# Kernel tuning notes

Hardware: AMD Instinct MI355X
Metric: run time of the kernel (lower is better)

## Reference

```python
import jax, jax.numpy as jnp
import numpy as np

C = 32
H = 8

def _layernorm(x, scale, bias, eps=1e-5):
    mu = jnp.mean(x, axis=-1, keepdims=True)
    var = jnp.mean(jnp.square(x - mu), axis=-1, keepdims=True)
    return (x - mu) * jax.lax.rsqrt(var + eps) * scale + bias


def setup_inputs() -> dict:
    key = jax.random.key(0)
    ks = jax.random.split(key, 10)
    B, s, i, j = 1, 128, 256, 256
    m = jax.random.normal(ks[0], (B, s, i, C), dtype=jnp.float32)
    z = jax.random.normal(ks[1], (B, i, j, C), dtype=jnp.float32)
    sd = 1.0 / np.sqrt(C)
    return {
        "m": m,
        "z": z,
        "ln_scale": jnp.ones((C,), jnp.float32),
        "ln_bias": jnp.zeros((C,), jnp.float32),
        "lnb_scale": jnp.ones((C,), jnp.float32),
        "lnb_bias": jnp.zeros((C,), jnp.float32),
        "wq": jax.random.normal(ks[2], (C, C * H), jnp.float32) * sd,
        "wk": jax.random.normal(ks[3], (C, C * H), jnp.float32) * sd,
        "wv": jax.random.normal(ks[4], (C, C * H), jnp.float32) * sd,
        "wb": jax.random.normal(ks[5], (C, H), jnp.float32) * sd,
        "wg": jax.random.normal(ks[6], (C, C * H), jnp.float32) * sd,
        "wo": jax.random.normal(ks[7], (C * H, C), jnp.float32) * (1.0 / np.sqrt(C * H)),
        "bo": jnp.zeros((C,), jnp.float32),
    }


def reference(m, z, ln_scale, ln_bias, lnb_scale, lnb_bias, wq, wk, wv, wb, wg, wo, bo):
    B, s, i, _ = m.shape
    j = z.shape[2]
    mn = _layernorm(m, ln_scale, ln_bias)                      # (B,s,i,c)
    q = (mn @ wq).reshape(B, s, i, H, C)                        # (B,s,i,h,c)
    k = (mn @ wk).reshape(B, s, i, H, C)
    v = (mn @ wv).reshape(B, s, i, H, C)
    gate = jax.nn.sigmoid(mn @ wg).reshape(B, s, i, H, C)       # (B,s,i,h,c)
    b = (_layernorm(z, lnb_scale, lnb_bias) @ wb)               # (B,i,j,h)
    a = jnp.einsum('bsihc,bsjhc->bsijh', q, k) * (C ** -0.5) + b[:, None]
    a = jax.nn.softmax(a, axis=-2)                              # softmax over j
    o = gate * jnp.einsum('bsijh,bsjhc->bsihc', a, v)
    o = o.reshape(B, s, i, H * C)
    return o @ wo + bo
```

## Files before the change

kernel.cpp:

```cpp
#include <hip/hip_runtime.h>

constexpr int NC = 32;
constexpr int NH = 8;
constexpr int NS = 128;
constexpr int NI = 256;
constexpr int NJ = 256;
constexpr float LN_EPS = 1e-5f;
constexpr float QSCALE = 0.17677669529663687f;
constexpr float LOG2E  = 1.4426950408889634f;

typedef __bf16 bf16x8 __attribute__((ext_vector_type(8)));
typedef __bf16 bf16x2 __attribute__((ext_vector_type(2)));
typedef float floatx4 __attribute__((ext_vector_type(4)));

__device__ __forceinline__ float fexp2(float x) {
#if __has_builtin(__builtin_amdgcn_exp2f)
    return __builtin_amdgcn_exp2f(x);
#else
    return exp2f(x);
#endif
}
__device__ __forceinline__ float frcp(float x) {
#if __has_builtin(__builtin_amdgcn_rcpf)
    return __builtin_amdgcn_rcpf(x);
#else
    return 1.0f / x;
#endif
}
__device__ __forceinline__ unsigned pk2c(float a, float b) {
    union { bf16x2 v; unsigned u; } c;
    c.v = bf16x2{(__bf16)a, (__bf16)b};
    return c.u;
}

__device__ __forceinline__ int qkOff(int row, int chunk) {
    return row * 32 + ((chunk ^ ((row >> 1) & 3)) << 3);
}
__device__ __forceinline__ int vOff(int c, int chunk) {
    return c * 256 + ((chunk ^ (c & 7)) << 3);
}
__device__ __forceinline__ int pOff(int wbase, int row, int chunk) {
    return wbase + row * 32 + ((chunk ^ ((row >> 1) & 3)) << 3);
}

__global__ __launch_bounds__(256) void biasprep_kernel(
    const float* __restrict__ z, const float* __restrict__ lnb_s,
    const float* __restrict__ lnb_b, const float* __restrict__ wb,
    const float* __restrict__ wq, const float* __restrict__ wk,
    const float* __restrict__ wv, const float* __restrict__ wg,
    const float* __restrict__ wo,
    float* __restrict__ bias32, unsigned short* __restrict__ wprep,
    unsigned short* __restrict__ wofrag)
{
    const int b = blockIdx.x;
    const int t = threadIdx.x;
    if (b < 256) {
        __shared__ float zL[256 * 33];
        const float4* src = (const float4*)(z + (size_t)b * NJ * NC);
#pragma unroll
        for (int k = 0; k < 8; ++k) {
            int idx = t + 256 * k;
            float4 v = src[idx];
            int f = idx * 4;
            int j = f >> 5, c = f & 31;
            zL[j * 33 + c]     = v.x; zL[j * 33 + c + 1] = v.y;
            zL[j * 33 + c + 2] = v.z; zL[j * 33 + c + 3] = v.w;
        }
        __syncthreads();

        float x[NC];
#pragma unroll
        for (int c = 0; c < NC; ++c) x[c] = zL[t * 33 + c];
        float mu = 0.f;
#pragma unroll
        for (int c = 0; c < NC; ++c) mu += x[c];
        mu *= (1.0f / NC);
        float var = 0.f;
#pragma unroll
        for (int c = 0; c < NC; ++c) { float d = x[c] - mu; var += d * d; }
        var *= (1.0f / NC);
        float rs = rsqrtf(var + LN_EPS);
        float acc[NH];
#pragma unroll
        for (int h = 0; h < NH; ++h) acc[h] = 0.f;
#pragma unroll
        for (int c = 0; c < NC; ++c) {
            float xn = (x[c] - mu) * rs * lnb_s[c] + lnb_b[c];
#pragma unroll
            for (int h = 0; h < NH; ++h) acc[h] += xn * wb[c * NH + h];
        }
        const int i = b;
        const int w_ = i >> 6, it = (i >> 4) & 3, lm = i & 15;
        const int jc = t >> 5, jt = (t >> 4) & 1, lq = (t >> 2) & 3, r = t & 3;
        const int base = jc * 8192 + w_ * 2048 + (jt * 4 + it) * 256
                       + (lq * 16 + lm) * 4 + r;
#pragma unroll
        for (int h = 0; h < NH; ++h)
            bias32[h * 65536 + base] = acc[h] * LOG2E;
    } else if (b < 272) {
        int g = (b - 256) * 256 + t;
        int p  = g >> 10;
        int h  = (g >> 7) & 7;
        int ct = (g >> 6) & 1;
        int l  = g & 63;
        const float* W = (p == 0) ? wq : (p == 1) ? wk : (p == 2) ? wv : wg;
        float scale = (p == 0) ? QSCALE * LOG2E : (p == 3) ? LOG2E : 1.0f;
        int col = 32 * h + 16 * ct + (l & 15);
        int r0  = 8 * (l >> 4);
        float v[8];
#pragma unroll
        for (int e = 0; e < 8; ++e) v[e] = W[(r0 + e) * 256 + col] * scale;
        uint4 u;
        u.x = pk2c(v[0], v[1]); u.y = pk2c(v[2], v[3]);
        u.z = pk2c(v[4], v[5]); u.w = pk2c(v[6], v[7]);
        *(uint4*)&wprep[g * 8] = u;
    } else {
        int g = (b - 272) * 256 + t;
        int tile = g >> 6;
        int l = g & 63;
        int kt = tile >> 1, nt = tile & 1;
        int r0 = kt * 32 + 8 * (l >> 4);
        int col = nt * 16 + (l & 15);
        float v[8];
#pragma unroll
        for (int e = 0; e < 8; ++e) v[e] = wo[(r0 + e) * 32 + col];
        uint4 u;
        u.x = pk2c(v[0], v[1]); u.y = pk2c(v[2], v[3]);
        u.z = pk2c(v[4], v[5]); u.w = pk2c(v[6], v[7]);
        *(uint4*)&wofrag[g * 8] = u;
    }
}

__global__ __launch_bounds__(256, 4) void attn_kernel(
    const float* __restrict__ m, const float* __restrict__ ln_s,
    const float* __restrict__ ln_b,
    const unsigned short* __restrict__ wprep,
    const float* __restrict__ bias32,
    unsigned short* __restrict__ attn16)
{
    __shared__ unsigned short KX[256 * 32];
    __shared__ unsigned short Vt[32 * 256];
    __shared__ unsigned short Pbuf[4 * 512];

    const int t = threadIdx.x;
    const int h = blockIdx.x & 7;
    const int s = blockIdx.x >> 3;
    const int l = t & 63, w = t >> 6;
    const int lm = l & 15, lq = l >> 4;
    const int ibase = w * 64;
    const int pwb = w * 512;
    const floatx4 zero = {0.f, 0.f, 0.f, 0.f};

    {
        const float4* mr = (const float4*)(m + ((size_t)s * NI + t) * NC);
        float x[NC];
#pragma unroll
        for (int k = 0; k < 8; ++k) {
            float4 v = mr[k];
            x[4*k] = v.x; x[4*k+1] = v.y; x[4*k+2] = v.z; x[4*k+3] = v.w;
        }
        float mu = 0.f;
#pragma unroll
        for (int c = 0; c < NC; ++c) mu += x[c];
        mu *= (1.0f / NC);
        float var = 0.f;
#pragma unroll
        for (int c = 0; c < NC; ++c) { float d = x[c] - mu; var += d * d; }
        var *= (1.0f / NC);
        float rs = rsqrtf(var + LN_EPS);
#pragma unroll
        for (int k = 0; k < 4; ++k) {
            uint4 u;
            u.x = pk2c((x[8*k+0]-mu)*rs*ln_s[8*k+0]+ln_b[8*k+0],
                       (x[8*k+1]-mu)*rs*ln_s[8*k+1]+ln_b[8*k+1]);
            u.y = pk2c((x[8*k+2]-mu)*rs*ln_s[8*k+2]+ln_b[8*k+2],
                       (x[8*k+3]-mu)*rs*ln_s[8*k+3]+ln_b[8*k+3]);
            u.z = pk2c((x[8*k+4]-mu)*rs*ln_s[8*k+4]+ln_b[8*k+4],
                       (x[8*k+5]-mu)*rs*ln_s[8*k+5]+ln_b[8*k+5]);
            u.w = pk2c((x[8*k+6]-mu)*rs*ln_s[8*k+6]+ln_b[8*k+6],
                       (x[8*k+7]-mu)*rs*ln_s[8*k+7]+ln_b[8*k+7]);
            *(uint4*)&KX[qkOff(t, k)] = u;
        }
    }

    const unsigned short* wp = wprep + ((size_t)h * 128 + l) * 8;
    bf16x8 wfQ[2], wfK[2], wfV[2];
#pragma unroll
    for (int ct = 0; ct < 2; ++ct) {
        wfQ[ct] = *(const bf16x8*)&wp[(0 * 1024 + ct * 64) * 8];
        wfK[ct] = *(const bf16x8*)&wp[(1 * 1024 + ct * 64) * 8];
        wfV[ct] = *(const bf16x8*)&wp[(2 * 1024 + ct * 64) * 8];
    }
    bf16x8 Xb[4];
#pragma unroll
    for (int it = 0; it < 4; ++it)
        Xb[it] = *(const bf16x8*)&KX[qkOff(ibase + it * 16 + lm, lq)];

#pragma unroll
    for (int it = 0; it < 4; ++it)
#pragma unroll
        for (int ct = 0; ct < 2; ++ct) {
            floatx4 d = __builtin_amdgcn_mfma_f32_16x16x32_bf16(wfQ[ct], Xb[it], zero, 0, 0, 0);
            uint2 u; u.x = pk2c(d[0], d[1]); u.y = pk2c(d[2], d[3]);
            int row = ibase + it * 16 + lm;
            *(uint2*)&KX[qkOff(row, 2 * ct + (lq >> 1)) + (lq & 1) * 4] = u;
        }
    bf16x8 Qb[4];
#pragma unroll
    for (int it = 0; it < 4; ++it)
        Qb[it] = *(const bf16x8*)&KX[qkOff(ibase + it * 16 + lm, lq)];

#pragma unroll
    for (int it = 0; it < 4; ++it)
#pragma unroll
        for (int ct = 0; ct < 2; ++ct) {
            floatx4 d = __builtin_amdgcn_mfma_f32_16x16x32_bf16(wfK[ct], Xb[it], zero, 0, 0, 0);
            uint2 u; u.x = pk2c(d[0], d[1]); u.y = pk2c(d[2], d[3]);
            int row = ibase + it * 16 + lm;
            *(uint2*)&KX[qkOff(row, 2 * ct + (lq >> 1)) + (lq & 1) * 4] = u;
        }

#pragma unroll
    for (int jt = 0; jt < 4; ++jt)
#pragma unroll
        for (int ct = 0; ct < 2; ++ct) {
            floatx4 d = __builtin_amdgcn_mfma_f32_16x16x32_bf16(Xb[jt], wfV[ct], zero, 0, 0, 0);
            uint2 u; u.x = pk2c(d[0], d[1]); u.y = pk2c(d[2], d[3]);
            int c = ct * 16 + lm;
            int chunk = 8 * w + 2 * jt + (lq >> 1);
            *(uint2*)&Vt[vOff(c, chunk) + (lq & 1) * 4] = u;
        }

    __syncthreads();

    floatx4 accO[2][4];
#pragma unroll
    for (int ct = 0; ct < 2; ++ct)
#pragma unroll
        for (int it = 0; it < 4; ++it) accO[ct][it] = zero;
    float accLv[4] = {0.f, 0.f, 0.f, 0.f};

    const float* bptr = bias32 + (size_t)h * 65536 + w * 2048 + l * 4;

    for (int jc = 0; jc < 8; ++jc) {
        const float* bj = bptr + jc * 8192;
        bf16x8 Ka0 = *(const bf16x8*)&KX[qkOff(jc * 32 + lm, lq)];
        bf16x8 Ka1 = *(const bf16x8*)&KX[qkOff(jc * 32 + 16 + lm, lq)];
        bf16x8 Va0 = *(const bf16x8*)&Vt[vOff(lm, 4 * jc + lq)];
        bf16x8 Va1 = *(const bf16x8*)&Vt[vOff(16 + lm, 4 * jc + lq)];
#pragma unroll
        for (int it = 0; it < 4; ++it) {
            floatx4 C0 = *(const floatx4*)(bj + it * 256);
            floatx4 S0 = __builtin_amdgcn_mfma_f32_16x16x32_bf16(Ka0, Qb[it], C0, 0, 0, 0);
            floatx4 C1 = *(const floatx4*)(bj + (4 + it) * 256);
            floatx4 S1 = __builtin_amdgcn_mfma_f32_16x16x32_bf16(Ka1, Qb[it], C1, 0, 0, 0);
            float p0 = fexp2(S0[0]), p1 = fexp2(S0[1]);
            float p2 = fexp2(S0[2]), p3 = fexp2(S0[3]);
            float p4 = fexp2(S1[0]), p5 = fexp2(S1[1]);
            float p6 = fexp2(S1[2]), p7 = fexp2(S1[3]);
            accLv[it] += ((p0 + p1) + (p2 + p3)) + ((p4 + p5) + (p6 + p7));
            uint2 u0; u0.x = pk2c(p0, p1); u0.y = pk2c(p2, p3);
            uint2 u1; u1.x = pk2c(p4, p5); u1.y = pk2c(p6, p7);
            *(uint2*)&Pbuf[pOff(pwb, lm, 0 + (lq >> 1)) + (lq & 1) * 4] = u0;
            *(uint2*)&Pbuf[pOff(pwb, lm, 2 + (lq >> 1)) + (lq & 1) * 4] = u1;
            bf16x8 Pb = *(const bf16x8*)&Pbuf[pOff(pwb, lm, lq)];
            accO[0][it] = __builtin_amdgcn_mfma_f32_16x16x32_bf16(Va0, Pb, accO[0][it], 0, 0, 0);
            accO[1][it] = __builtin_amdgcn_mfma_f32_16x16x32_bf16(Va1, Pb, accO[1][it], 0, 0, 0);
        }
    }

    {
        bf16x8 wfG0 = *(const bf16x8*)&wp[(3 * 1024 + 0 * 64) * 8];
        bf16x8 wfG1 = *(const bf16x8*)&wp[(3 * 1024 + 1 * 64) * 8];
#pragma unroll
        for (int it = 0; it < 4; ++it) {
            float L = accLv[it];
            L += __shfl_xor(L, 16, 64);
            L += __shfl_xor(L, 32, 64);
            const float inv = frcp(L);
            floatx4 d0 = __builtin_amdgcn_mfma_f32_16x16x32_bf16(wfG0, Xb[it], zero, 0, 0, 0);
            floatx4 d1 = __builtin_amdgcn_mfma_f32_16x16x32_bf16(wfG1, Xb[it], zero, 0, 0, 0);
            const size_t rowb = ((size_t)s * NI + ibase + it * 16 + lm) * 256 + h * 32;
            {
                float o0 = accO[0][it][0] * inv * frcp(1.0f + fexp2(-d0[0]));
                float o1 = accO[0][it][1] * inv * frcp(1.0f + fexp2(-d0[1]));
                float o2 = accO[0][it][2] * inv * frcp(1.0f + fexp2(-d0[2]));
                float o3 = accO[0][it][3] * inv * frcp(1.0f + fexp2(-d0[3]));
                uint2 u; u.x = pk2c(o0, o1); u.y = pk2c(o2, o3);
                *(uint2*)&attn16[rowb + 0 * 16 + lq * 4] = u;
            }
            {
                float o0 = accO[1][it][0] * inv * frcp(1.0f + fexp2(-d1[0]));
                float o1 = accO[1][it][1] * inv * frcp(1.0f + fexp2(-d1[1]));
                float o2 = accO[1][it][2] * inv * frcp(1.0f + fexp2(-d1[2]));
                float o3 = accO[1][it][3] * inv * frcp(1.0f + fexp2(-d1[3]));
                uint2 u; u.x = pk2c(o0, o1); u.y = pk2c(o2, o3);
                *(uint2*)&attn16[rowb + 1 * 16 + lq * 4] = u;
            }
        }
    }
}

__global__ __launch_bounds__(256) void proj_kernel(
    const unsigned short* __restrict__ attn16,
    const unsigned short* __restrict__ wofrag,
    const float* __restrict__ bo, float* __restrict__ out)
{
    const int t = threadIdx.x;
    const int l = t & 63, w = t >> 6;
    const int lm = l & 15, lq = l >> 4;
    const int row0 = blockIdx.x * 128 + w * 32;
    const floatx4 zero = {0.f, 0.f, 0.f, 0.f};

    floatx4 acc[2][2];
#pragma unroll
    for (int it = 0; it < 2; ++it)
#pragma unroll
        for (int nt = 0; nt < 2; ++nt) acc[it][nt] = zero;

#pragma unroll 2
    for (int kt = 0; kt < 8; ++kt) {
        bf16x8 a0 = *(const bf16x8*)&attn16[(size_t)(row0 + lm) * 256 + kt * 32 + lq * 8];
        bf16x8 a1 = *(const bf16x8*)&attn16[(size_t)(row0 + 16 + lm) * 256 + kt * 32 + lq * 8];
        bf16x8 b0 = *(const bf16x8*)&wofrag[((kt * 2 + 0) * 64 + l) * 8];
        bf16x8 b1 = *(const bf16x8*)&wofrag[((kt * 2 + 1) * 64 + l) * 8];
        acc[0][0] = __builtin_amdgcn_mfma_f32_16x16x32_bf16(a0, b0, acc[0][0], 0, 0, 0);
        acc[0][1] = __builtin_amdgcn_mfma_f32_16x16x32_bf16(a0, b1, acc[0][1], 0, 0, 0);
        acc[1][0] = __builtin_amdgcn_mfma_f32_16x16x32_bf16(a1, b0, acc[1][0], 0, 0, 0);
        acc[1][1] = __builtin_amdgcn_mfma_f32_16x16x32_bf16(a1, b1, acc[1][1], 0, 0, 0);
    }

    float bov[2] = {bo[lm], bo[16 + lm]};
#pragma unroll
    for (int it = 0; it < 2; ++it)
#pragma unroll
        for (int nt = 0; nt < 2; ++nt)
#pragma unroll
            for (int r = 0; r < 4; ++r)
                out[(size_t)(row0 + it * 16 + lq * 4 + r) * NC + nt * 16 + lm]
                    = acc[it][nt][r] + bov[nt];
}

extern "C" void kernel_launch(void* const* d_in, const int* in_sizes, int n_in,
                              void* d_out, int out_size, void* d_ws, size_t ws_size,
                              hipStream_t stream) {
    const float* m     = (const float*)d_in[0];
    const float* z     = (const float*)d_in[1];
    const float* ln_s  = (const float*)d_in[2];
    const float* ln_b  = (const float*)d_in[3];
    const float* lnb_s = (const float*)d_in[4];
    const float* lnb_b = (const float*)d_in[5];
    const float* wq    = (const float*)d_in[6];
    const float* wk    = (const float*)d_in[7];
    const float* wv    = (const float*)d_in[8];
    const float* wb    = (const float*)d_in[9];
    const float* wg    = (const float*)d_in[10];
    const float* wo    = (const float*)d_in[11];
    const float* bo    = (const float*)d_in[12];
    float* out = (float*)d_out;

    float* bias32 = (float*)d_ws;
    unsigned short* wprep  = (unsigned short*)((char*)d_ws + (2u << 20));
    unsigned short* wofrag = (unsigned short*)((char*)d_ws + (2u << 20) + 65536);
    unsigned short* attn16 = (unsigned short*)((char*)d_ws + (2u << 20) + 65536 + 16384);

    biasprep_kernel<<<276, 256, 0, stream>>>(z, lnb_s, lnb_b, wb, wq, wk, wv, wg,
                                             wo, bias32, wprep, wofrag);
    attn_kernel<<<NS * NH, 256, 0, stream>>>(m, ln_s, ln_b, wprep, bias32, attn16);
    proj_kernel<<<(NS * NI) / 128, 256, 0, stream>>>(attn16, wofrag, bo, out);
}
```

Baseline: 123.6 us.

## Split bias prep finer, enlarge P buffer, unroll j loop, shrink proj tiles

Result: slower. 140.1 us (+13.4%).

```diff
diff --git a/kernel.cpp b/kernel.cpp
--- a/kernel.cpp
+++ b/kernel.cpp
@@ -39,8 +39,8 @@
 __device__ __forceinline__ int vOff(int c, int chunk) {
     return c * 256 + ((chunk ^ (c & 7)) << 3);
 }
-__device__ __forceinline__ int pOff(int wbase, int row, int chunk) {
-    return wbase + row * 32 + ((chunk ^ ((row >> 1) & 3)) << 3);
+__device__ __forceinline__ int pOff(int base, int row, int chunk) {
+    return base + row * 32 + ((chunk ^ ((row >> 1) & 3)) << 3);
 }
 
 __global__ __launch_bounds__(256) void biasprep_kernel(
@@ -54,23 +54,27 @@
 {
     const int b = blockIdx.x;
     const int t = threadIdx.x;
-    if (b < 256) {
-        __shared__ float zL[256 * 33];
-        const float4* src = (const float4*)(z + (size_t)b * NJ * NC);
-#pragma unroll
-        for (int k = 0; k < 8; ++k) {
+    if (b < 1024) {
+        __shared__ float zL[64 * 33];
+        const int i  = b >> 2;
+        const int jq = b & 3;
+        const float4* src = (const float4*)(z + ((size_t)i * NJ + jq * 64) * NC);
+#pragma unroll
+        for (int k = 0; k < 2; ++k) {
             int idx = t + 256 * k;
             float4 v = src[idx];
             int f = idx * 4;
-            int j = f >> 5, c = f & 31;
-            zL[j * 33 + c]     = v.x; zL[j * 33 + c + 1] = v.y;
-            zL[j * 33 + c + 2] = v.z; zL[j * 33 + c + 3] = v.w;
+            int jr = f >> 5, c = f & 31;
+            zL[jr * 33 + c]     = v.x; zL[jr * 33 + c + 1] = v.y;
+            zL[jr * 33 + c + 2] = v.z; zL[jr * 33 + c + 3] = v.w;
         }
         __syncthreads();
 
+        const int jr = t & 63;
+        const int h0 = t >> 6;
         float x[NC];
 #pragma unroll
-        for (int c = 0; c < NC; ++c) x[c] = zL[t * 33 + c];
+        for (int c = 0; c < NC; ++c) x[c] = zL[jr * 33 + c];
         float mu = 0.f;
 #pragma unroll
         for (int c = 0; c < NC; ++c) mu += x[c];
@@ -80,25 +84,22 @@
         for (int c = 0; c < NC; ++c) { float d = x[c] - mu; var += d * d; }
         var *= (1.0f / NC);
         float rs = rsqrtf(var + LN_EPS);
-        float acc[NH];
-#pragma unroll
-        for (int h = 0; h < NH; ++h) acc[h] = 0.f;
+        float a0 = 0.f, a1 = 0.f;
 #pragma unroll
         for (int c = 0; c < NC; ++c) {
             float xn = (x[c] - mu) * rs * lnb_s[c] + lnb_b[c];
-#pragma unroll
-            for (int h = 0; h < NH; ++h) acc[h] += xn * wb[c * NH + h];
-        }
-        const int i = b;
-        const int w_ = i >> 6, it = (i >> 4) & 3, lm = i & 15;
-        const int jc = t >> 5, jt = (t >> 4) & 1, lq = (t >> 2) & 3, r = t & 3;
-        const int base = jc * 8192 + w_ * 2048 + (jt * 4 + it) * 256
-                       + (lq * 16 + lm) * 4 + r;
-#pragma unroll
-        for (int h = 0; h < NH; ++h)
-            bias32[h * 65536 + base] = acc[h] * LOG2E;
-    } else if (b < 272) {
-        int g = (b - 256) * 256 + t;
+            a0 += xn * wb[c * NH + h0];
+            a1 += xn * wb[c * NH + h0 + 4];
+        }
+        const int j  = jq * 64 + jr;
+        const int w_ = i >> 6, it_ = (i >> 4) & 3, lm_ = i & 15;
+        const int jcb = j >> 5, jt = (j >> 4) & 1, lqb = (j >> 2) & 3, rb = j & 3;
+        const int base = jcb * 8192 + w_ * 2048 + (jt * 4 + it_) * 256
+                       + (lqb * 16 + lm_) * 4 + rb;
+        bias32[h0 * 65536 + base]       = a0 * LOG2E;
+        bias32[(h0 + 4) * 65536 + base] = a1 * LOG2E;
+    } else if (b < 1040) {
+        int g = (b - 1024) * 256 + t;
         int p  = g >> 10;
         int h  = (g >> 7) & 7;
         int ct = (g >> 6) & 1;
@@ -115,7 +116,7 @@
         u.z = pk2c(v[4], v[5]); u.w = pk2c(v[6], v[7]);
         *(uint4*)&wprep[g * 8] = u;
     } else {
-        int g = (b - 272) * 256 + t;
+        int g = (b - 1040) * 256 + t;
         int tile = g >> 6;
         int l = g & 63;
         int kt = tile >> 1, nt = tile & 1;
@@ -131,7 +132,7 @@
     }
 }
 
-__global__ __launch_bounds__(256, 4) void attn_kernel(
+__global__ __launch_bounds__(256, 3) void attn_kernel(
     const float* __restrict__ m, const float* __restrict__ ln_s,
     const float* __restrict__ ln_b,
     const unsigned short* __restrict__ wprep,
@@ -140,7 +141,7 @@
 {
     __shared__ unsigned short KX[256 * 32];
     __shared__ unsigned short Vt[32 * 256];
-    __shared__ unsigned short Pbuf[4 * 512];
+    __shared__ unsigned short Pbuf[4 * 2048];
 
     const int t = threadIdx.x;
     const int h = blockIdx.x & 7;
@@ -148,7 +149,7 @@
     const int l = t & 63, w = t >> 6;
     const int lm = l & 15, lq = l >> 4;
     const int ibase = w * 64;
-    const int pwb = w * 512;
+    const int pwb = w * 2048;
     const floatx4 zero = {0.f, 0.f, 0.f, 0.f};
 
     {
@@ -242,6 +243,7 @@
 
     const float* bptr = bias32 + (size_t)h * 65536 + w * 2048 + l * 4;
 
+#pragma unroll 2
     for (int jc = 0; jc < 8; ++jc) {
         const float* bj = bptr + jc * 8192;
         bf16x8 Ka0 = *(const bf16x8*)&KX[qkOff(jc * 32 + lm, lq)];
@@ -250,6 +252,7 @@
         bf16x8 Va1 = *(const bf16x8*)&Vt[vOff(16 + lm, 4 * jc + lq)];
 #pragma unroll
         for (int it = 0; it < 4; ++it) {
+            const int pb = pwb + it * 512;
             floatx4 C0 = *(const floatx4*)(bj + it * 256);
             floatx4 S0 = __builtin_amdgcn_mfma_f32_16x16x32_bf16(Ka0, Qb[it], C0, 0, 0, 0);
             floatx4 C1 = *(const floatx4*)(bj + (4 + it) * 256);
@@ -261,9 +264,9 @@
             accLv[it] += ((p0 + p1) + (p2 + p3)) + ((p4 + p5) + (p6 + p7));
             uint2 u0; u0.x = pk2c(p0, p1); u0.y = pk2c(p2, p3);
             uint2 u1; u1.x = pk2c(p4, p5); u1.y = pk2c(p6, p7);
-            *(uint2*)&Pbuf[pOff(pwb, lm, 0 + (lq >> 1)) + (lq & 1) * 4] = u0;
-            *(uint2*)&Pbuf[pOff(pwb, lm, 2 + (lq >> 1)) + (lq & 1) * 4] = u1;
-            bf16x8 Pb = *(const bf16x8*)&Pbuf[pOff(pwb, lm, lq)];
+            *(uint2*)&Pbuf[pOff(pb, lm, 0 + (lq >> 1)) + (lq & 1) * 4] = u0;
+            *(uint2*)&Pbuf[pOff(pb, lm, 2 + (lq >> 1)) + (lq & 1) * 4] = u1;
+            bf16x8 Pb = *(const bf16x8*)&Pbuf[pOff(pb, lm, lq)];
             accO[0][it] = __builtin_amdgcn_mfma_f32_16x16x32_bf16(Va0, Pb, accO[0][it], 0, 0, 0);
             accO[1][it] = __builtin_amdgcn_mfma_f32_16x16x32_bf16(Va1, Pb, accO[1][it], 0, 0, 0);
         }
@@ -309,36 +312,27 @@
     const int t = threadIdx.x;
     const int l = t & 63, w = t >> 6;
     const int lm = l & 15, lq = l >> 4;
-    const int row0 = blockIdx.x * 128 + w * 32;
+    const int row0 = blockIdx.x * 64 + w * 16;
     const floatx4 zero = {0.f, 0.f, 0.f, 0.f};
 
-    floatx4 acc[2][2];
-#pragma unroll
-    for (int it = 0; it < 2; ++it)
-#pragma unroll
-        for (int nt = 0; nt < 2; ++nt) acc[it][nt] = zero;
-
-#pragma unroll 2
+    floatx4 acc[2] = {zero, zero};
+
+#pragma unroll
     for (int kt = 0; kt < 8; ++kt) {
         bf16x8 a0 = *(const bf16x8*)&attn16[(size_t)(row0 + lm) * 256 + kt * 32 + lq * 8];
-        bf16x8 a1 = *(const bf16x8*)&attn16[(size_t)(row0 + 16 + lm) * 256 + kt * 32 + lq * 8];
         bf16x8 b0 = *(const bf16x8*)&wofrag[((kt * 2 + 0) * 64 + l) * 8];
         bf16x8 b1 = *(const bf16x8*)&wofrag[((kt * 2 + 1) * 64 + l) * 8];
-        acc[0][0] = __builtin_amdgcn_mfma_f32_16x16x32_bf16(a0, b0, acc[0][0], 0, 0, 0);
-        acc[0][1] = __builtin_amdgcn_mfma_f32_16x16x32_bf16(a0, b1, acc[0][1], 0, 0, 0);
-        acc[1][0] = __builtin_amdgcn_mfma_f32_16x16x32_bf16(a1, b0, acc[1][0], 0, 0, 0);
-        acc[1][1] = __builtin_amdgcn_mfma_f32_16x16x32_bf16(a1, b1, acc[1][1], 0, 0, 0);
+        acc[0] = __builtin_amdgcn_mfma_f32_16x16x32_bf16(a0, b0, acc[0], 0, 0, 0);
+        acc[1] = __builtin_amdgcn_mfma_f32_16x16x32_bf16(a0, b1, acc[1], 0, 0, 0);
     }
 
     float bov[2] = {bo[lm], bo[16 + lm]};
 #pragma unroll
-    for (int it = 0; it < 2; ++it)
-#pragma unroll
-        for (int nt = 0; nt < 2; ++nt)
-#pragma unroll
-            for (int r = 0; r < 4; ++r)
-                out[(size_t)(row0 + it * 16 + lq * 4 + r) * NC + nt * 16 + lm]
-                    = acc[it][nt][r] + bov[nt];
+    for (int nt = 0; nt < 2; ++nt)
+#pragma unroll
+        for (int r = 0; r < 4; ++r)
+            out[(size_t)(row0 + lq * 4 + r) * NC + nt * 16 + lm]
+                = acc[nt][r] + bov[nt];
 }
 
 extern "C" void kernel_launch(void* const* d_in, const int* in_sizes, int n_in,
@@ -364,8 +358,8 @@
     unsigned short* wofrag = (unsigned short*)((char*)d_ws + (2u << 20) + 65536);
     unsigned short* attn16 = (unsigned short*)((char*)d_ws + (2u << 20) + 65536 + 16384);
 
-    biasprep_kernel<<<276, 256, 0, stream>>>(z, lnb_s, lnb_b, wb, wq, wk, wv, wg,
-                                             wo, bias32, wprep, wofrag);
+    biasprep_kernel<<<1044, 256, 0, stream>>>(z, lnb_s, lnb_b, wb, wq, wk, wv, wg,
+                                              wo, bias32, wprep, wofrag);
     attn_kernel<<<NS * NH, 256, 0, stream>>>(m, ln_s, ln_b, wprep, bias32, attn16);
-    proj_kernel<<<(NS * NI) / 128, 256, 0, stream>>>(attn16, wofrag, bo, out);
-}
+    proj_kernel<<<(NS * NI) / 64, 256, 0, stream>>>(attn16, wofrag, bo, out);
+}
```
